# Kernel optimization log

Hardware: AMD Instinct MI355X
Metric: run time of the kernel (lower is better)

The kernel has to match this reference:

```python
import jax, jax.numpy as jnp
import numpy as np

N_NODES = 20000
N_EDGES = 320000
H = 4        # heads
C = 64       # channels per head
D = H * C    # 256, also input_dim
L = 4        # num_layers
NEG_SLOPE = 0.2


def setup_inputs() -> dict:
    key = jax.random.key(0)
    ks = jax.random.split(key, 8)
    x = jax.random.normal(ks[0], (N_NODES, D), jnp.float32)
    edge_index = jax.random.randint(ks[1], (2, N_EDGES), 0, N_NODES, dtype=jnp.int64)
    Ws = jax.random.normal(ks[2], (L, D, D), jnp.float32) * 0.05
    att_src = jax.random.normal(ks[3], (L, H, C), jnp.float32) * 0.05
    att_dst = jax.random.normal(ks[4], (L, H, C), jnp.float32) * 0.05
    biases = jax.random.normal(ks[5], (L, D), jnp.float32) * 0.05
    Wout = jax.random.normal(ks[6], (D, D), jnp.float32) * 0.05
    bout = jax.random.normal(ks[7], (D,), jnp.float32) * 0.05
    return {"x": x, "edge_index": edge_index, "Ws": Ws, "att_src": att_src,
            "att_dst": att_dst, "biases": biases, "Wout": Wout, "bout": bout}


def reference(x, edge_index, Ws, att_src, att_dst, biases, Wout, bout):
    n = x.shape[0]
    # PyG GATConv adds self-loops by default; same edge set each layer.
    loops = jnp.arange(n, dtype=edge_index.dtype)
    src = jnp.concatenate([edge_index[0], loops])  # message sources
    dst = jnp.concatenate([edge_index[1], loops])  # message targets (softmax groups)
    h = x
    for l in range(L):
        hp = (h @ Ws[l]).reshape(n, H, C)                      # [N,H,C]
        a_s = jnp.einsum('nhc,hc->nh', hp, att_src[l])          # [N,H]
        a_d = jnp.einsum('nhc,hc->nh', hp, att_dst[l])          # [N,H]
        e = jax.nn.leaky_relu(a_s[src] + a_d[dst], NEG_SLOPE)   # [E',H]
        # per-destination segment softmax (every node has a self-loop -> non-empty)
        m = jax.ops.segment_max(e, dst, num_segments=n)         # [N,H]
        ex = jnp.exp(e - m[dst])
        denom = jax.ops.segment_sum(ex, dst, num_segments=n)    # [N,H]
        alpha = ex / denom[dst]                                 # [E',H]
        msg = hp[src] * alpha[:, :, None]                       # [E',H,C]
        h = jax.ops.segment_sum(msg, dst, num_segments=n).reshape(n, D) + biases[l]
        h = jax.nn.elu(h)  # dropout is identity in eval mode
    g = jnp.mean(h, axis=0, keepdims=True)                      # mean pooling, single graph
    return g @ Wout + bout                                      # [1, D]
```

## Files before the change

### kernel.cpp

```cpp
#include <hip/hip_runtime.h>
#include <hip/hip_bf16.h>

#define H 4
#define C 64
#define D 256
#define NEG_SLOPE 0.2f
#define ESHIFT 8.0f
#define AGGC 48

typedef _Float16 half_t;
typedef __attribute__((ext_vector_type(8))) _Float16 half8v;
typedef __attribute__((ext_vector_type(4))) float f32x4;


__device__ inline void fma_mix_pair(float& clo, float& chi, unsigned wu, float a) {
    asm("v_fma_mix_f32 %0, %2, %3, %0 op_sel_hi:[1,0,0]\n\t"
        "v_fma_mix_f32 %1, %2, %3, %1 op_sel:[1,0,0] op_sel_hi:[1,0,0]"
        : "+v"(clo), "+v"(chi)
        : "v"(wu), "v"(a));
}

__global__ void count_kernel(const int* __restrict__ ei, int E, int N, int* __restrict__ counts) {
    int i = blockIdx.x * blockDim.x + threadIdx.x;
    if (i >= E + N) return;
    int d = (i < E) ? ei[E + i] : (i - E);
    atomicAdd(&counts[d], 1);
}

__global__ __launch_bounds__(1024) void scan1(const int* __restrict__ counts,
                                              int* __restrict__ row_ptr,
                                              int* __restrict__ bsum, int N) {
    __shared__ int wsum[16];
    int tid = threadIdx.x, lane = tid & 63, wid = tid >> 6;
    int idx = blockIdx.x * 1024 + tid;
    int v = (idx < N) ? counts[idx] : 0;
    int val = v;
    #pragma unroll
    for (int o = 1; o < 64; o <<= 1) {
        int t = __shfl_up(val, o);
        if (lane >= o) val += t;
    }
    if (lane == 63) wsum[wid] = val;
    __syncthreads();
    int woff = 0;
    #pragma unroll
    for (int w = 0; w < 16; w++) woff += (w < wid) ? wsum[w] : 0;
    if (idx < N) row_ptr[idx] = woff + val - v;
    if (tid == 1023) bsum[blockIdx.x] = woff + val;
}

__global__ void scan2(int* __restrict__ bsum, int* __restrict__ row_ptr, int nb, int N) {
    int lane = threadIdx.x;
    int v = (lane < nb) ? bsum[lane] : 0;
    int val = v;
    #pragma unroll
    for (int o = 1; o < 64; o <<= 1) {
        int t = __shfl_up(val, o);
        if (lane >= o) val += t;
    }
    if (lane < nb) bsum[lane] = val - v;
    if (lane == 63) row_ptr[N] = val;
}

__global__ __launch_bounds__(1024) void scan3(int* __restrict__ row_ptr,
                                              const int* __restrict__ bsum,
                                              int* __restrict__ cursor, int N) {
    int idx = blockIdx.x * 1024 + threadIdx.x;
    if (idx >= N) return;
    int r = row_ptr[idx] + bsum[blockIdx.x];
    row_ptr[idx] = r;
    cursor[idx] = r;
}

__global__ void scatter_kernel(const int* __restrict__ ei, int E, int N,
                               int* __restrict__ cursor, int* __restrict__ csr_src) {
    int i = blockIdx.x * blockDim.x + threadIdx.x;
    if (i >= E + N) return;
    int s, d;
    if (i < E) { s = ei[i]; d = ei[E + i]; }
    else       { s = d = i - E; }
    int pos = atomicAdd(&cursor[d], 1);
    csr_src[pos] = s;
}

__global__ void conv_x(const float* __restrict__ in, half_t* __restrict__ xt, int total) {
    int t = blockIdx.x * blockDim.x + threadIdx.x;
    if (t >= total) return;
    int i = t >> 5, o = t & 31;
    const float* src = in + (size_t)i * 256 + o * 8;
    float4 v0 = *(const float4*)src;
    float4 v1 = *(const float4*)(src + 4);
    half_t q[8] __attribute__((aligned(16)));
    q[0] = (half_t)v0.x; q[1] = (half_t)v0.y; q[2] = (half_t)v0.z; q[3] = (half_t)v0.w;
    q[4] = (half_t)v1.x; q[5] = (half_t)v1.y; q[6] = (half_t)v1.z; q[7] = (half_t)v1.w;
    size_t dst = (size_t)(i >> 4) * 4096 + (o >> 2) * 512 + (o & 3) * 128 + (i & 15) * 8;
    *(half8v*)(xt + dst) = *(half8v*)q;
}

__global__ void conv_w(const float* __restrict__ W, half_t* __restrict__ wt, int total) {
    int idx = blockIdx.x * blockDim.x + threadIdx.x;
    if (idx >= total) return;
    int Lr = idx & 63;
    int s  = (idx >> 6) & 7;
    int cb = (idx >> 9) & 3;
    int h  = (idx >> 11) & 3;
    int l  = idx >> 13;
    int col = h * 64 + cb * 16 + (Lr & 15);
    int k0  = 32 * s + (Lr >> 4) * 8;
    half_t q[8] __attribute__((aligned(16)));
    #pragma unroll
    for (int j = 0; j < 8; j++)
        q[j] = (half_t)W[(size_t)l * 65536 + (size_t)(k0 + j) * 256 + col];
    *(half8v*)(wt + (size_t)idx * 8) = *(half8v*)q;
}

__global__ __launch_bounds__(256) void gemm_f16(
    const half_t* __restrict__ At, const half_t* __restrict__ Wt,
    const float* __restrict__ asrc, const float* __restrict__ adst,
    half_t* __restrict__ hp, float* __restrict__ as_out, float* __restrict__ ad_out,
    int Npad) {
    __shared__ float sp[4][4][16], sd[4][4][16];
    int nwg = gridDim.x;
    int bq = nwg >> 3, br = nwg & 7;
    int xcd = blockIdx.x & 7, bidx = blockIdx.x >> 3;
    int swz = (xcd < br ? xcd * (bq + 1) : br * (bq + 1) + (xcd - br) * bq) + bidx;
    int cb = threadIdx.x >> 6, lane = threadIdx.x & 63;
    int h = swz & 3, pg = swz >> 2;
    int rlo = lane & 15, q = lane >> 4;
    const half_t* pb = Wt + (size_t)h * 16384 + (size_t)cb * 4096 + lane * 8;

    half8v B[8];
    #pragma unroll
    for (int s = 0; s < 8; s++) B[s] = *(const half8v*)(pb + s * 512);

    float av = asrc[h * 64 + cb * 16 + rlo];
    float dv = adst[h * 64 + cb * 16 + rlo];
    half_t* hph = hp + (size_t)h * Npad * 64;

    #pragma unroll
    for (int pp = 0; pp < 4; pp++) {
        int p = pg * 4 + pp;
        const half_t* pa = At + (size_t)p * 4096 + lane * 8;

        f32x4 acc = (f32x4){0.f, 0.f, 0.f, 0.f};
        half8v A0 = *(const half8v*)(pa);
        half8v A1;
        #pragma unroll
        for (int s = 0; s < 8; s += 2) {
            A1 = *(const half8v*)(pa + (s + 1) * 512);
            acc = __builtin_amdgcn_mfma_f32_16x16x32_f16(A0, B[s], acc, 0, 0, 0);
            if (s < 6) A0 = *(const half8v*)(pa + (s + 2) * 512);
            acc = __builtin_amdgcn_mfma_f32_16x16x32_f16(A1, B[s + 1], acc, 0, 0, 0);
        }

        int grow = p * 16 + q * 4;
        #pragma unroll
        for (int i = 0; i < 4; i++)
            hph[(size_t)(grow + i) * 64 + cb * 16 + rlo] = (half_t)acc[i];

        float ps[4], pd[4];
        #pragma unroll
        for (int i = 0; i < 4; i++) { ps[i] = acc[i] * av; pd[i] = acc[i] * dv; }
        #pragma unroll
        for (int mask = 1; mask <= 8; mask <<= 1) {
            #pragma unroll
            for (int i = 0; i < 4; i++) {
                ps[i] += __shfl_xor(ps[i], mask);
                pd[i] += __shfl_xor(pd[i], mask);
            }
        }
        if (rlo == 0) {
            #pragma unroll
            for (int i = 0; i < 4; i++) {
                sp[pp][cb][q * 4 + i] = ps[i];
                sd[pp][cb][q * 4 + i] = pd[i];
            }
        }
    }
    __syncthreads();
    if (threadIdx.x < 64) {
        int pp = threadIdx.x >> 4, r = threadIdx.x & 15;
        float s_ = sp[pp][0][r] + sp[pp][1][r] + sp[pp][2][r] + sp[pp][3][r];
        float d_ = sd[pp][0][r] + sd[pp][1][r] + sd[pp][2][r] + sd[pp][3][r];
        int grow = (pg * 4 + pp) * 16 + r;
        as_out[(size_t)grow * 4 + h] = s_;
        ad_out[(size_t)grow * 4 + h] = d_;
    }
}

#define AGG_BODY(g)                                                          \
    {                                                                        \
        int e_ = 2 * (g) + es;                                               \
        int s_ = __float_as_int(pk[wv][nn][e_][0]);                          \
        float a_ = pk[wv][nn][e_][1];                                        \
        const uint4 w_ = *(const uint4*)(hpb + (size_t)s_ * 64);             \
        asum += a_;                                                          \
        fma_mix_pair(c0, c1, w_.x, a_);                                      \
        fma_mix_pair(c2, c3, w_.y, a_);                                      \
        fma_mix_pair(c4, c5, w_.z, a_);                                      \
        fma_mix_pair(c6, c7, w_.w, a_);                                      \
    }

__global__ __launch_bounds__(256) void gat_aggregate(
    const half_t* __restrict__ hp, const float* __restrict__ as_, const float* __restrict__ ad_,
    const int* __restrict__ row_ptr, const int* __restrict__ csr_src,
    const float* __restrict__ bias, half_t* __restrict__ hnext,
    int N, int Npad, int ngroups) {
    __shared__ float pk[4][4][AGGC][2];
    int wv = threadIdx.x >> 6, lane = threadIdx.x & 63;
    int h = blockIdx.x / ngroups;
    int db = (blockIdx.x % ngroups) * 16;
    int nn = lane >> 4;
    int d = db + wv * 4 + nn;
    if (d >= N) return;
    int r0 = row_ptr[d], deg = row_ptr[d + 1] - r0;
    float adv = ad_[(size_t)d * 4 + h];
    const half_t* hph = hp + (size_t)h * Npad * 64;

    if (deg <= AGGC) {
        int le = lane & 15;
        #pragma unroll
        for (int k = 0; k < 3; k++) {
            int e = k * 16 + le;
            if (e < deg) {
                int s = csr_src[r0 + e];
                float ev = as_[(size_t)s * 4 + h] + adv;
                ev = ev > 0.f ? ev : NEG_SLOPE * ev;
                pk[wv][nn][e][0] = __int_as_float(s);
                pk[wv][nn][e][1] = __expf(ev - ESHIFT);
            }
        }
        int es = (lane >> 3) & 1, chq = lane & 7;
        const half_t* hpb = hph + chq * 8;
        float c0 = 0.f, c1 = 0.f, c2 = 0.f, c3 = 0.f;
        float c4 = 0.f, c5 = 0.f, c6 = 0.f, c7 = 0.f;
        float asum = 0.f;
        int full = deg >> 1;
        int g = 0;
        for (; g + 4 <= full; g += 4) {
            AGG_BODY(g) AGG_BODY(g + 1) AGG_BODY(g + 2) AGG_BODY(g + 3)
        }
        for (; g < full; g++) { AGG_BODY(g) }
        if ((deg & 1) && es == 0) {
            int e_ = deg - 1;
            int s_ = __float_as_int(pk[wv][nn][e_][0]);
            float a_ = pk[wv][nn][e_][1];
            const uint4 w_ = *(const uint4*)(hpb + (size_t)s_ * 64);
            asum += a_;
            fma_mix_pair(c0, c1, w_.x, a_);
            fma_mix_pair(c2, c3, w_.y, a_);
            fma_mix_pair(c4, c5, w_.z, a_);
            fma_mix_pair(c6, c7, w_.w, a_);
        }
        c0 += __shfl_xor(c0, 8); c1 += __shfl_xor(c1, 8);
        c2 += __shfl_xor(c2, 8); c3 += __shfl_xor(c3, 8);
        c4 += __shfl_xor(c4, 8); c5 += __shfl_xor(c5, 8);
        c6 += __shfl_xor(c6, 8); c7 += __shfl_xor(c7, 8);
        asum += __shfl_xor(asum, 8);
        if (es == 0) {
            float inv = 1.0f / asum;
            int o = h * 8 + chq;
            const float* bp = bias + h * 64 + chq * 8;
            float vv[8] = {c0, c1, c2, c3, c4, c5, c6, c7};
            half_t oh[8] __attribute__((aligned(16)));
            #pragma unroll
            for (int j = 0; j < 8; j++) {
                float v = vv[j] * inv + bp[j];
                v = v > 0.f ? v : (__expf(v) - 1.0f);
                oh[j] = (half_t)v;
            }
            size_t dst = (size_t)(d >> 4) * 4096 + (o >> 2) * 512 + (o & 3) * 128 + (d & 15) * 8;
            *(half8v*)(hnext + dst) = *(half8v*)oh;
        }
    } else {
        int lc = lane & 15;
        float cA = 0.f, cB = 0.f, cC = 0.f, cD = 0.f, asum = 0.f;
        for (int i = 0; i < deg; i++) {
            int s = csr_src[r0 + i];
            float ev = as_[(size_t)s * 4 + h] + adv;
            ev = ev > 0.f ? ev : NEG_SLOPE * ev;
            float a = __expf(ev - ESHIFT);
            asum += a;
            const uint2 w = *(const uint2*)(hph + (size_t)s * 64 + lc * 4);
            fma_mix_pair(cA, cB, w.x, a);
            fma_mix_pair(cC, cD, w.y, a);
        }
        float inv = 1.0f / asum;
        int c = h * 64 + lc * 4;
        float vv[4] = {cA, cB, cC, cD};
        half_t oh[4] __attribute__((aligned(8)));
        #pragma unroll
        for (int j = 0; j < 4; j++) {
            float v = vv[j] * inv + bias[c + j];
            v = v > 0.f ? v : (__expf(v) - 1.0f);
            oh[j] = (half_t)v;
        }
        size_t dst = (size_t)(d >> 4) * 4096 + (c >> 5) * 512 + ((c >> 3) & 3) * 128 + (d & 15) * 8 + (c & 7);
        *(uint2*)(hnext + dst) = *(uint2*)oh;
    }
}

__global__ __launch_bounds__(256) void col_sum_f16(const half_t* __restrict__ hin,
                                                   float* __restrict__ partial, int N, int rows_per_blk) {
    int c = threadIdx.x;
    int r0 = blockIdx.x * rows_per_blk;
    int r1 = min(r0 + rows_per_blk, N);
    int coff = (c >> 5) * 512 + ((c >> 3) & 3) * 128 + (c & 7);
    float acc = 0.f;
    for (int r = r0; r < r1; r++)
        acc += (float)hin[(size_t)(r >> 4) * 4096 + coff + (r & 15) * 8];
    partial[(size_t)blockIdx.x * 256 + c] = acc;
}

__global__ __launch_bounds__(256) void final_kernel(const float* __restrict__ partial,
                                                    const float* __restrict__ Wout,
                                                    const float* __restrict__ bout,
                                                    float* __restrict__ out, float invN, int nb) {
    __shared__ float gl[256];
    int j = threadIdx.x;
    float s = 0.f;
    for (int b = 0; b < nb; b++) s += partial[(size_t)b * 256 + j];
    gl[j] = s;
    __syncthreads();
    float acc = 0.f;
    for (int i = 0; i < 256; i++) acc += gl[i] * Wout[i * 256 + j];
    out[j] = acc * invN + bout[j];
}

extern "C" void kernel_launch(void* const* d_in, const int* in_sizes, int n_in,
                              void* d_out, int out_size, void* d_ws, size_t ws_size,
                              hipStream_t stream) {
    const float* x       = (const float*)d_in[0];
    const int*   ei      = (const int*)d_in[1];
    const float* Ws      = (const float*)d_in[2];
    const float* att_src = (const float*)d_in[3];
    const float* att_dst = (const float*)d_in[4];
    const float* biases  = (const float*)d_in[5];
    const float* Wout    = (const float*)d_in[6];
    const float* bout    = (const float*)d_in[7];
    float* out = (float*)d_out;

    int N = in_sizes[0] / D;
    int E = in_sizes[1] / 2;
    int L = in_sizes[2] / (D * D);
    int Etot = E + N;
    int Npad = (N + 63) & ~63;

    char* ws = (char*)d_ws;
    size_t off = 0;
    auto alloc = [&](size_t bytes) -> void* {
        void* p = ws + off;
        off = (off + bytes + 255) & ~(size_t)255;
        return p;
    };
    half_t* xt     = (half_t*)alloc((size_t)Npad * D * 2);
    half_t* hp     = (half_t*)alloc((size_t)Npad * D * 2);
    float* a_s     = (float*)alloc((size_t)Npad * H * 4);
    float* a_d     = (float*)alloc((size_t)Npad * H * 4);
    half_t* wt     = (half_t*)alloc((size_t)L * D * D * 2);
    int*   counts  = (int*)alloc((size_t)N * 4);
    int*   row_ptr = (int*)alloc((size_t)(N + 1) * 4);
    int*   cursor  = (int*)alloc((size_t)N * 4);
    int*   bsum    = (int*)alloc(64 * 4);
    int*   csr_src = (int*)alloc((size_t)Etot * 4);
    int rows_per_blk = 254;
    int nb_pool = (N + rows_per_blk - 1) / rows_per_blk;
    float* partial = (float*)alloc((size_t)nb_pool * 256 * 4);
    if (off > ws_size) return;

    int thr = 256;

    int xtot = N * 32;
    conv_x<<<(xtot + thr - 1) / thr, thr, 0, stream>>>(x, xt, xtot);
    int wtot = L * 4 * 4 * 8 * 64;
    conv_w<<<(wtot + thr - 1) / thr, thr, 0, stream>>>(Ws, wt, wtot);

    hipMemsetAsync(counts, 0, (size_t)N * 4, stream);
    count_kernel<<<(Etot + thr - 1) / thr, thr, 0, stream>>>(ei, E, N, counts);
    int nb_scan = (N + 1023) / 1024;
    scan1<<<nb_scan, 1024, 0, stream>>>(counts, row_ptr, bsum, N);
    scan2<<<1, 64, 0, stream>>>(bsum, row_ptr, nb_scan, N);
    scan3<<<nb_scan, 1024, 0, stream>>>(row_ptr, bsum, cursor, N);
    scatter_kernel<<<(Etot + thr - 1) / thr, thr, 0, stream>>>(ei, E, N, cursor, csr_src);

    int gemm_blocks = (Npad / 64) * 4;
    int ngroups = (N + 15) / 16;
    int agg_blocks = 4 * ngroups;
    for (int l = 0; l < L; l++) {
        gemm_f16<<<gemm_blocks, 256, 0, stream>>>(
            xt, wt + (size_t)l * D * D,
            att_src + (size_t)l * H * C, att_dst + (size_t)l * H * C,
            hp, a_s, a_d, Npad);
        gat_aggregate<<<agg_blocks, 256, 0, stream>>>(
            hp, a_s, a_d, row_ptr, csr_src, biases + (size_t)l * D, xt, N, Npad, ngroups);
    }

    col_sum_f16<<<nb_pool, thr, 0, stream>>>(xt, partial, N, rows_per_blk);
    final_kernel<<<1, thr, 0, stream>>>(partial, Wout, bout, out, 1.0f / (float)N, nb_pool);
}
```

Before: 264.8 us.

## Store projected features as fp8 and fold scan/memset kernels

New measurement: 269.2 us. About the same (+1.6%).

```diff
diff --git a/kernel.cpp b/kernel.cpp
--- a/kernel.cpp
+++ b/kernel.cpp
@@ -11,14 +11,8 @@
 typedef _Float16 half_t;
 typedef __attribute__((ext_vector_type(8))) _Float16 half8v;
 typedef __attribute__((ext_vector_type(4))) float f32x4;
-
-
-__device__ inline void fma_mix_pair(float& clo, float& chi, unsigned wu, float a) {
-    asm("v_fma_mix_f32 %0, %2, %3, %0 op_sel_hi:[1,0,0]\n\t"
-        "v_fma_mix_f32 %1, %2, %3, %1 op_sel:[1,0,0] op_sel_hi:[1,0,0]"
-        : "+v"(clo), "+v"(chi)
-        : "v"(wu), "v"(a));
-}
+typedef __attribute__((ext_vector_type(2))) float f32x2;
+
 
 __global__ void count_kernel(const int* __restrict__ ei, int E, int N, int* __restrict__ counts) {
     int i = blockIdx.x * blockDim.x + threadIdx.x;
@@ -49,25 +43,24 @@
     if (tid == 1023) bsum[blockIdx.x] = woff + val;
 }
 
-__global__ void scan2(int* __restrict__ bsum, int* __restrict__ row_ptr, int nb, int N) {
-    int lane = threadIdx.x;
-    int v = (lane < nb) ? bsum[lane] : 0;
-    int val = v;
-    #pragma unroll
-    for (int o = 1; o < 64; o <<= 1) {
-        int t = __shfl_up(val, o);
-        if (lane >= o) val += t;
-    }
-    if (lane < nb) bsum[lane] = val - v;
-    if (lane == 63) row_ptr[N] = val;
-}
-
 __global__ __launch_bounds__(1024) void scan3(int* __restrict__ row_ptr,
                                               const int* __restrict__ bsum,
-                                              int* __restrict__ cursor, int N) {
+                                              int* __restrict__ cursor, int N, int nb) {
+    __shared__ int woff_s;
+    if (threadIdx.x == 0) {
+        int w = 0;
+        for (int i = 0; i < blockIdx.x; i++) w += bsum[i];
+        woff_s = w;
+        if (blockIdx.x == 0) {
+            int tot = 0;
+            for (int i = 0; i < nb; i++) tot += bsum[i];
+            row_ptr[N] = tot;
+        }
+    }
+    __syncthreads();
     int idx = blockIdx.x * 1024 + threadIdx.x;
     if (idx >= N) return;
-    int r = row_ptr[idx] + bsum[blockIdx.x];
+    int r = row_ptr[idx] + woff_s;
     row_ptr[idx] = r;
     cursor[idx] = r;
 }
@@ -83,8 +76,10 @@
     csr_src[pos] = s;
 }
 
-__global__ void conv_x(const float* __restrict__ in, half_t* __restrict__ xt, int total) {
+__global__ void conv_x(const float* __restrict__ in, half_t* __restrict__ xt, int total,
+                       int* __restrict__ counts, int N) {
     int t = blockIdx.x * blockDim.x + threadIdx.x;
+    if (t < N) counts[t] = 0;
     if (t >= total) return;
     int i = t >> 5, o = t & 31;
     const float* src = in + (size_t)i * 256 + o * 8;
@@ -117,7 +112,7 @@
 __global__ __launch_bounds__(256) void gemm_f16(
     const half_t* __restrict__ At, const half_t* __restrict__ Wt,
     const float* __restrict__ asrc, const float* __restrict__ adst,
-    half_t* __restrict__ hp, float* __restrict__ as_out, float* __restrict__ ad_out,
+    unsigned char* __restrict__ hp, float* __restrict__ as_out, float* __restrict__ ad_out,
     int Npad) {
     __shared__ float sp[4][4][16], sd[4][4][16];
     int nwg = gridDim.x;
@@ -135,7 +130,7 @@
 
     float av = asrc[h * 64 + cb * 16 + rlo];
     float dv = adst[h * 64 + cb * 16 + rlo];
-    half_t* hph = hp + (size_t)h * Npad * 64;
+    unsigned char* hph = hp + (size_t)h * Npad * 64;
 
     #pragma unroll
     for (int pp = 0; pp < 4; pp++) {
@@ -154,9 +149,11 @@
         }
 
         int grow = p * 16 + q * 4;
+        unsigned pk0 = __builtin_amdgcn_cvt_pk_fp8_f32(acc[0], acc[1], 0, 0);
+        pk0 = __builtin_amdgcn_cvt_pk_fp8_f32(acc[2], acc[3], pk0, 1);
         #pragma unroll
         for (int i = 0; i < 4; i++)
-            hph[(size_t)(grow + i) * 64 + cb * 16 + rlo] = (half_t)acc[i];
+            hph[(size_t)(grow + i) * 64 + cb * 16 + rlo] = (unsigned char)((pk0 >> (8 * i)) & 0xFF);
 
         float ps[4], pd[4];
         #pragma unroll
@@ -188,21 +185,25 @@
     }
 }
 
-#define AGG_BODY(g)                                                          \
-    {                                                                        \
-        int e_ = 2 * (g) + es;                                               \
-        int s_ = __float_as_int(pk[wv][nn][e_][0]);                          \
-        float a_ = pk[wv][nn][e_][1];                                        \
-        const uint4 w_ = *(const uint4*)(hpb + (size_t)s_ * 64);             \
-        asum += a_;                                                          \
-        fma_mix_pair(c0, c1, w_.x, a_);                                      \
-        fma_mix_pair(c2, c3, w_.y, a_);                                      \
-        fma_mix_pair(c4, c5, w_.z, a_);                                      \
-        fma_mix_pair(c6, c7, w_.w, a_);                                      \
+#define AGG_BODY(g)                                                           \
+    {                                                                         \
+        int e_ = 2 * (g) + es;                                                \
+        int s_ = __float_as_int(pk[wv][nn][e_][0]);                           \
+        float a_ = pk[wv][nn][e_][1];                                         \
+        const uint2 w_ = *(const uint2*)(hpb + (size_t)s_ * 64);              \
+        f32x2 f0 = __builtin_amdgcn_cvt_pk_f32_fp8(w_.x, 0);                  \
+        f32x2 f1 = __builtin_amdgcn_cvt_pk_f32_fp8(w_.x, 1);                  \
+        f32x2 f2 = __builtin_amdgcn_cvt_pk_f32_fp8(w_.y, 0);                  \
+        f32x2 f3 = __builtin_amdgcn_cvt_pk_f32_fp8(w_.y, 1);                  \
+        asum += a_;                                                           \
+        c0 = fmaf(f0.x, a_, c0); c1 = fmaf(f0.y, a_, c1);                     \
+        c2 = fmaf(f1.x, a_, c2); c3 = fmaf(f1.y, a_, c3);                     \
+        c4 = fmaf(f2.x, a_, c4); c5 = fmaf(f2.y, a_, c5);                     \
+        c6 = fmaf(f3.x, a_, c6); c7 = fmaf(f3.y, a_, c7);                     \
     }
 
 __global__ __launch_bounds__(256) void gat_aggregate(
-    const half_t* __restrict__ hp, const float* __restrict__ as_, const float* __restrict__ ad_,
+    const unsigned char* __restrict__ hp, const float* __restrict__ as_, const float* __restrict__ ad_,
     const int* __restrict__ row_ptr, const int* __restrict__ csr_src,
     const float* __restrict__ bias, half_t* __restrict__ hnext,
     int N, int Npad, int ngroups) {
@@ -215,7 +216,7 @@
     if (d >= N) return;
     int r0 = row_ptr[d], deg = row_ptr[d + 1] - r0;
     float adv = ad_[(size_t)d * 4 + h];
-    const half_t* hph = hp + (size_t)h * Npad * 64;
+    const unsigned char* hph = hp + (size_t)h * Npad * 64;
 
     if (deg <= AGGC) {
         int le = lane & 15;
@@ -231,7 +232,7 @@
             }
         }
         int es = (lane >> 3) & 1, chq = lane & 7;
-        const half_t* hpb = hph + chq * 8;
+        const unsigned char* hpb = hph + chq * 8;
         float c0 = 0.f, c1 = 0.f, c2 = 0.f, c3 = 0.f;
         float c4 = 0.f, c5 = 0.f, c6 = 0.f, c7 = 0.f;
         float asum = 0.f;
@@ -245,12 +246,16 @@
             int e_ = deg - 1;
             int s_ = __float_as_int(pk[wv][nn][e_][0]);
             float a_ = pk[wv][nn][e_][1];
-            const uint4 w_ = *(const uint4*)(hpb + (size_t)s_ * 64);
+            const uint2 w_ = *(const uint2*)(hpb + (size_t)s_ * 64);
+            f32x2 f0 = __builtin_amdgcn_cvt_pk_f32_fp8(w_.x, 0);
+            f32x2 f1 = __builtin_amdgcn_cvt_pk_f32_fp8(w_.x, 1);
+            f32x2 f2 = __builtin_amdgcn_cvt_pk_f32_fp8(w_.y, 0);
+            f32x2 f3 = __builtin_amdgcn_cvt_pk_f32_fp8(w_.y, 1);
             asum += a_;
-            fma_mix_pair(c0, c1, w_.x, a_);
-            fma_mix_pair(c2, c3, w_.y, a_);
-            fma_mix_pair(c4, c5, w_.z, a_);
-            fma_mix_pair(c6, c7, w_.w, a_);
+            c0 = fmaf(f0.x, a_, c0); c1 = fmaf(f0.y, a_, c1);
+            c2 = fmaf(f1.x, a_, c2); c3 = fmaf(f1.y, a_, c3);
+            c4 = fmaf(f2.x, a_, c4); c5 = fmaf(f2.y, a_, c5);
+            c6 = fmaf(f3.x, a_, c6); c7 = fmaf(f3.y, a_, c7);
         }
         c0 += __shfl_xor(c0, 8); c1 += __shfl_xor(c1, 8);
         c2 += __shfl_xor(c2, 8); c3 += __shfl_xor(c3, 8);
@@ -281,9 +286,11 @@
             ev = ev > 0.f ? ev : NEG_SLOPE * ev;
             float a = __expf(ev - ESHIFT);
             asum += a;
-            const uint2 w = *(const uint2*)(hph + (size_t)s * 64 + lc * 4);
-            fma_mix_pair(cA, cB, w.x, a);
-            fma_mix_pair(cC, cD, w.y, a);
+            unsigned w = *(const unsigned*)(hph + (size_t)s * 64 + lc * 4);
+            f32x2 g0 = __builtin_amdgcn_cvt_pk_f32_fp8(w, 0);
+            f32x2 g1 = __builtin_amdgcn_cvt_pk_f32_fp8(w, 1);
+            cA = fmaf(g0.x, a, cA); cB = fmaf(g0.y, a, cB);
+            cC = fmaf(g1.x, a, cC); cD = fmaf(g1.y, a, cD);
         }
         float inv = 1.0f / asum;
         int c = h * 64 + lc * 4;
@@ -353,16 +360,16 @@
         off = (off + bytes + 255) & ~(size_t)255;
         return p;
     };
-    half_t* xt     = (half_t*)alloc((size_t)Npad * D * 2);
-    half_t* hp     = (half_t*)alloc((size_t)Npad * D * 2);
-    float* a_s     = (float*)alloc((size_t)Npad * H * 4);
-    float* a_d     = (float*)alloc((size_t)Npad * H * 4);
-    half_t* wt     = (half_t*)alloc((size_t)L * D * D * 2);
-    int*   counts  = (int*)alloc((size_t)N * 4);
-    int*   row_ptr = (int*)alloc((size_t)(N + 1) * 4);
-    int*   cursor  = (int*)alloc((size_t)N * 4);
-    int*   bsum    = (int*)alloc(64 * 4);
-    int*   csr_src = (int*)alloc((size_t)Etot * 4);
+    half_t* xt         = (half_t*)alloc((size_t)Npad * D * 2);
+    unsigned char* hp  = (unsigned char*)alloc((size_t)Npad * D);
+    float* a_s         = (float*)alloc((size_t)Npad * H * 4);
+    float* a_d         = (float*)alloc((size_t)Npad * H * 4);
+    half_t* wt         = (half_t*)alloc((size_t)L * D * D * 2);
+    int*   counts      = (int*)alloc((size_t)N * 4);
+    int*   row_ptr     = (int*)alloc((size_t)(N + 1) * 4);
+    int*   cursor      = (int*)alloc((size_t)N * 4);
+    int*   bsum        = (int*)alloc(64 * 4);
+    int*   csr_src     = (int*)alloc((size_t)Etot * 4);
     int rows_per_blk = 254;
     int nb_pool = (N + rows_per_blk - 1) / rows_per_blk;
     float* partial = (float*)alloc((size_t)nb_pool * 256 * 4);
@@ -371,16 +378,14 @@
     int thr = 256;
 
     int xtot = N * 32;
-    conv_x<<<(xtot + thr - 1) / thr, thr, 0, stream>>>(x, xt, xtot);
+    conv_x<<<(xtot + thr - 1) / thr, thr, 0, stream>>>(x, xt, xtot, counts, N);
     int wtot = L * 4 * 4 * 8 * 64;
     conv_w<<<(wtot + thr - 1) / thr, thr, 0, stream>>>(Ws, wt, wtot);
 
-    hipMemsetAsync(counts, 0, (size_t)N * 4, stream);
     count_kernel<<<(Etot + thr - 1) / thr, thr, 0, stream>>>(ei, E, N, counts);
     int nb_scan = (N + 1023) / 1024;
     scan1<<<nb_scan, 1024, 0, stream>>>(counts, row_ptr, bsum, N);
-    scan2<<<1, 64, 0, stream>>>(bsum, row_ptr, nb_scan, N);
-    scan3<<<nb_scan, 1024, 0, stream>>>(row_ptr, bsum, cursor, N);
+    scan3<<<nb_scan, 1024, 0, stream>>>(row_ptr, bsum, cursor, N, nb_scan);
     scatter_kernel<<<(Etot + thr - 1) / thr, thr, 0, stream>>>(ei, E, N, cursor, csr_src);
 
     int gemm_blocks = (Npad / 64) * 4;
```
